# Optimization experiments

Hardware: AMD Instinct MI355X
Metric: run time of the kernel (lower is better)

Reference implementation:

```python
import jax, jax.numpy as jnp
import numpy as np

BN_EPS = 1e-5


def bn_relu(x, gamma, beta):
    # x: [N, C, L]; BatchNorm1d train-mode: per-channel stats over (N, L), biased var
    mean = jnp.mean(x, axis=(0, 2), keepdims=True)
    var = jnp.mean(jnp.square(x - mean), axis=(0, 2), keepdims=True)
    xn = (x - mean) * jax.lax.rsqrt(var + BN_EPS)
    return jax.nn.relu(xn * gamma[None, :, None] + beta[None, :, None])


def setup_inputs() -> dict:
    key = jax.random.key(0)
    ks = jax.random.split(key, 10)
    N, C, L = 8, 512, 2048
    IC = C // 2
    s = 0.02
    return {
        "A": jax.random.normal(ks[0], (N, C, L), jnp.float32),
        "B": jax.random.normal(ks[1], (N, C, L), jnp.float32),
        "bn_gamma": jnp.ones((C,), jnp.float32),
        "bn_beta": jnp.zeros((C,), jnp.float32),
        "theta_w": jax.random.normal(ks[2], (C, IC), jnp.float32) * s,
        "theta_b": jax.random.normal(ks[3], (IC,), jnp.float32) * s,
        "phi_w": jax.random.normal(ks[4], (C, IC), jnp.float32) * s,
        "phi_b": jax.random.normal(ks[5], (IC,), jnp.float32) * s,
        "g_w": jax.random.normal(ks[6], (C, IC), jnp.float32) * s,
        "g_b": jax.random.normal(ks[7], (IC,), jnp.float32) * s,
        "W_w": jax.random.normal(ks[8], (IC, C), jnp.float32) * s,
        "W_b": jax.random.normal(ks[9], (C,), jnp.float32) * s,
    }


def reference(A, B, bn_gamma, bn_beta, theta_w, theta_b, phi_w, phi_b, g_w, g_b, W_w, W_b):
    # A, B: [N, C, L]
    An = bn_relu(A, bn_gamma, bn_beta).transpose(0, 2, 1)  # [N, L, C]
    Bn = bn_relu(B, bn_gamma, bn_beta).transpose(0, 2, 1)  # [N, L, C]

    q = An @ theta_w + theta_b                 # [N, L, IC]
    k = Bn @ phi_w + phi_b                     # [N, L, IC]
    v = An @ g_w + g_b                         # [N, L, IC]

    scores = jnp.einsum("bnc,bmc->bnm", q, k)  # [N, L, L]  (no scaling in source)
    attn = jax.nn.softmax(scores, axis=-1)
    y = jnp.einsum("bnm,bmc->bnc", attn, v)    # [N, L, IC]

    out = An + (y @ W_w + W_b)                 # residual, [N, L, C]
    return out.transpose(0, 2, 1)              # [N, C, L]
```

## Files before the change

### kernel.cpp

```cpp
#include <hip/hip_runtime.h>

using bf16 = __bf16;
typedef __attribute__((ext_vector_type(8))) __bf16 bf16x8;
typedef __attribute__((ext_vector_type(4))) __bf16 bf16x4;
typedef __attribute__((ext_vector_type(4))) float f32x4;
typedef __attribute__((ext_vector_type(16))) float f32x16;
typedef __attribute__((ext_vector_type(4))) unsigned u32x4;
typedef __attribute__((ext_vector_type(2))) unsigned u32x2;

#define NB 8
#define CC 512
#define LL 2048
#define IC 256
#define NLTOT 16384
#define NSPLIT 4
#define BATCH_STRIDE 524288

__device__ inline bf16 f2bf(float f) {
    unsigned u = __builtin_bit_cast(unsigned, f);
    unsigned r = (u + 0x7fff + ((u >> 16) & 1)) >> 16;
    return __builtin_bit_cast(bf16, (unsigned short)r);
}
__device__ inline unsigned packbf(float lo, float hi) {
    unsigned a = (unsigned)__builtin_bit_cast(unsigned short, f2bf(lo));
    unsigned b = (unsigned)__builtin_bit_cast(unsigned short, f2bf(hi));
    return (b << 16) | a;
}

typedef const __attribute__((address_space(1))) void gas_void;
typedef __attribute__((address_space(3))) void las_void;

static constexpr size_t oScale = 0;
static constexpr size_t oWT    = 8192;
static constexpr size_t oAn    = oWT + 4ull * 262144;
static constexpr size_t oBn    = oAn + 16777216ull;
static constexpr size_t oQ     = oBn + 16777216ull;
static constexpr size_t oK     = oQ + 8388608ull;
static constexpr size_t oVT    = oK + 8388608ull;
static constexpr size_t oY     = oVT + 8388608ull;
static constexpr size_t oProj  = oY + 8388608ull;

__global__ __launch_bounds__(256) void prep_weights(
    const float* __restrict__ theta_w, const float* __restrict__ phi_w,
    const float* __restrict__ g_w, const float* __restrict__ W_w,
    bf16* __restrict__ wts)
{
    int idx = blockIdx.x * 256 + threadIdx.x;
    int which = idx >> 17;
    int o = idx & 131071;
    float v;
    if (which < 3) {
        const float* W = which == 0 ? theta_w : (which == 1 ? phi_w : g_w);
        int ic = o >> 9, cc = o & 511;
        v = W[cc * IC + ic];
    } else {
        int cc = o >> 8, ic = o & 255;
        v = W_w[ic * CC + cc];
    }
    wts[(size_t)which * 131072 + o] = f2bf(v);
}

__global__ __launch_bounds__(256) void bn_stats(
    const float* __restrict__ A, const float* __restrict__ B,
    const float* __restrict__ gamma, const float* __restrict__ beta,
    float* __restrict__ scaleshift)
{
    int bid = blockIdx.x;
    int tensor = bid >> 9, c = bid & 511;
    const float* X = tensor ? B : A;
    int t = threadIdx.x;
    float s = 0.f, sq = 0.f;
    for (int n = 0; n < NB; ++n) {
        const float* row = &X[((size_t)(n * CC + c)) << 11];
        for (int j = t * 4; j < LL; j += 1024) {
            float4 v = *(const float4*)&row[j];
            s += v.x + v.y + v.z + v.w;
            sq += v.x * v.x + v.y * v.y + v.z * v.z + v.w * v.w;
        }
    }
    __shared__ float rs[256], rq[256];
    rs[t] = s; rq[t] = sq;
    __syncthreads();
    for (int step = 128; step > 0; step >>= 1) {
        if (t < step) { rs[t] += rs[t + step]; rq[t] += rq[t + step]; }
        __syncthreads();
    }
    if (t == 0) {
        float mean = rs[0] * (1.f / 16384.f);
        float var = rq[0] * (1.f / 16384.f) - mean * mean;
        float rsq = rsqrtf(var + 1e-5f);
        float sc = gamma[c] * rsq;
        scaleshift[tensor * 1024 + c] = sc;
        scaleshift[tensor * 1024 + 512 + c] = beta[c] - mean * sc;
    }
}

__global__ __launch_bounds__(256) void bn_apply_transpose(
    const float* __restrict__ X, const float* __restrict__ scale,
    const float* __restrict__ shift, bf16* __restrict__ Out)
{
    int bidx = blockIdx.x;
    int lt = bidx & 31, ct = (bidx >> 5) & 7, n = bidx >> 8;
    int c0 = ct * 64, l0 = lt * 64;
    __shared__ float tile[64][65];
    int t = threadIdx.x;
    #pragma unroll
    for (int i = 0; i < 4; ++i) {
        int r = i * 16 + (t >> 4);
        int c4 = (t & 15) * 4;
        float s = scale[c0 + r], sh = shift[c0 + r];
        float4 v = *(const float4*)&X[(((size_t)n * CC + c0 + r) << 11) + l0 + c4];
        tile[r][c4 + 0] = fmaxf(v.x * s + sh, 0.f);
        tile[r][c4 + 1] = fmaxf(v.y * s + sh, 0.f);
        tile[r][c4 + 2] = fmaxf(v.z * s + sh, 0.f);
        tile[r][c4 + 3] = fmaxf(v.w * s + sh, 0.f);
    }
    __syncthreads();
    #pragma unroll
    for (int i = 0; i < 2; ++i) {
        int lr = i * 32 + (t >> 3);
        int c8 = (t & 7) * 8;
        bf16 tmp[8];
        #pragma unroll
        for (int e = 0; e < 8; ++e) tmp[e] = f2bf(tile[c8 + e][lr]);
        *(bf16x8*)&Out[(((size_t)(n << 11)) + l0 + lr) * CC + c0 + c8] = *(bf16x8*)tmp;
    }
}

__global__ __launch_bounds__(256) void gemm_qkv(
    const bf16* __restrict__ An, const bf16* __restrict__ Bn,
    const bf16* __restrict__ wts,
    const float* __restrict__ theta_b, const float* __restrict__ phi_b,
    const float* __restrict__ g_b,
    bf16* __restrict__ qB, bf16* __restrict__ kB, bf16* __restrict__ vB)
{
    int bid = blockIdx.x;
    int which = bid >> 8;
    int sub = bid & 255;
    const bf16* A  = (which == 1) ? Bn : An;
    const bf16* BT = wts + (size_t)which * 131072;
    const float* bias = which == 0 ? theta_b : (which == 1 ? phi_b : g_b);
    bf16* dst = which == 0 ? qB : (which == 1 ? kB : vB);

    int tn = sub & 1, tm = sub >> 1;
    int m0 = tm * 128, n0 = tn * 128;
    __shared__ bf16 a_lds[128][72];
    __shared__ bf16 b_lds[128][72];
    int t = threadIdx.x;
    int l = t & 63, w = t >> 6;
    int wr = w >> 1, wc = w & 1;
    f32x4 acc[4][4] = {};
    for (int k0 = 0; k0 < CC; k0 += 64) {
        __syncthreads();
        #pragma unroll
        for (int i = 0; i < 4; ++i) {
            int ci = t + i * 256;
            int row = ci >> 3, c8 = (ci & 7) * 8;
            *(bf16x8*)&a_lds[row][c8] = *(const bf16x8*)&A[(size_t)(m0 + row) * CC + k0 + c8];
            *(bf16x8*)&b_lds[row][c8] = *(const bf16x8*)&BT[(size_t)(n0 + row) * CC + k0 + c8];
        }
        __syncthreads();
        #pragma unroll
        for (int ks = 0; ks < 2; ++ks) {
            bf16x8 af[4], bfr[4];
            #pragma unroll
            for (int mi = 0; mi < 4; ++mi)
                af[mi] = *(const bf16x8*)&a_lds[wr * 64 + mi * 16 + (l & 15)][ks * 32 + (l >> 4) * 8];
            #pragma unroll
            for (int ni = 0; ni < 4; ++ni)
                bfr[ni] = *(const bf16x8*)&b_lds[wc * 64 + ni * 16 + (l & 15)][ks * 32 + (l >> 4) * 8];
            #pragma unroll
            for (int mi = 0; mi < 4; ++mi)
                #pragma unroll
                for (int ni = 0; ni < 4; ++ni)
                    acc[mi][ni] = __builtin_amdgcn_mfma_f32_16x16x32_bf16(af[mi], bfr[ni], acc[mi][ni], 0, 0, 0);
        }
    }
    #pragma unroll
    for (int mi = 0; mi < 4; ++mi)
        #pragma unroll
        for (int ni = 0; ni < 4; ++ni) {
            int col = n0 + wc * 64 + ni * 16 + (l & 15);
            float bv = bias[col];
            int row0 = m0 + wr * 64 + mi * 16 + (l >> 4) * 4;
            int nb = row0 >> 11;
            int li0 = row0 & 2047;
            size_t base = (size_t)nb * BATCH_STRIDE + (size_t)(li0 >> 5) * 8192;
            if (which < 2) {
                size_t a0 = base + (col >> 3) * 256 + (li0 & 31) * 8 + (col & 7);
                #pragma unroll
                for (int r = 0; r < 4; ++r)
                    dst[a0 + r * 8] = f2bf(acc[mi][ni][r] + bv);
            } else {
                bf16 tmp[4];
                #pragma unroll
                for (int r = 0; r < 4; ++r) tmp[r] = f2bf(acc[mi][ni][r] + bv);
                int kvin = li0 & 31;
                int grp = ((col >> 5) << 2) | ((kvin >> 4) << 1) | ((kvin >> 3) & 1);
                *(bf16x4*)&dst[base + grp * 256 + (col & 31) * 8 + (kvin & 7)] = *(bf16x4*)tmp;
            }
        }
}

__global__ __launch_bounds__(256) void gemm_w(
    const bf16* __restrict__ A, const bf16* __restrict__ BT,
    const float* __restrict__ bias, float* __restrict__ Cout,
    int Nn, int K, int nTilesN)
{
    int bid = blockIdx.x;
    int tn = bid % nTilesN, tm = bid / nTilesN;
    int m0 = tm * 128, n0 = tn * 128;
    __shared__ bf16 a_lds[128][72];
    __shared__ bf16 b_lds[128][72];
    int t = threadIdx.x;
    int l = t & 63, w = t >> 6;
    int wr = w >> 1, wc = w & 1;
    f32x4 acc[4][4] = {};
    for (int k0 = 0; k0 < K; k0 += 64) {
        __syncthreads();
        #pragma unroll
        for (int i = 0; i < 4; ++i) {
            int ci = t + i * 256;
            int row = ci >> 3, c8 = (ci & 7) * 8;
            *(bf16x8*)&a_lds[row][c8] = *(const bf16x8*)&A[(size_t)(m0 + row) * K + k0 + c8];
            *(bf16x8*)&b_lds[row][c8] = *(const bf16x8*)&BT[(size_t)(n0 + row) * K + k0 + c8];
        }
        __syncthreads();
        #pragma unroll
        for (int ks = 0; ks < 2; ++ks) {
            bf16x8 af[4], bfr[4];
            #pragma unroll
            for (int mi = 0; mi < 4; ++mi)
                af[mi] = *(const bf16x8*)&a_lds[wr * 64 + mi * 16 + (l & 15)][ks * 32 + (l >> 4) * 8];
            #pragma unroll
            for (int ni = 0; ni < 4; ++ni)
                bfr[ni] = *(const bf16x8*)&b_lds[wc * 64 + ni * 16 + (l & 15)][ks * 32 + (l >> 4) * 8];
            #pragma unroll
            for (int mi = 0; mi < 4; ++mi)
                #pragma unroll
                for (int ni = 0; ni < 4; ++ni)
                    acc[mi][ni] = __builtin_amdgcn_mfma_f32_16x16x32_bf16(af[mi], bfr[ni], acc[mi][ni], 0, 0, 0);
        }
    }
    #pragma unroll
    for (int mi = 0; mi < 4; ++mi)
        #pragma unroll
        for (int ni = 0; ni < 4; ++ni) {
            int col = n0 + wc * 64 + ni * 16 + (l & 15);
            float bv = bias[col];
            #pragma unroll
            for (int r = 0; r < 4; ++r) {
                int row = m0 + wr * 64 + mi * 16 + (l >> 4) * 4 + r;
                Cout[(size_t)row * Nn + col] = acc[mi][ni][r] + bv;
            }
        }
}

__global__ __launch_bounds__(256, 2) void flash_attn32(
    const bf16* __restrict__ QB, const bf16* __restrict__ KB,
    const bf16* __restrict__ VB, bf16* __restrict__ part, float* __restrict__ ml)
{
    int bid = blockIdx.x;
    int nb = bid & 7;
    int split = (bid >> 3) & 3;
    int qt = bid >> 5;
    int t = threadIdx.x, l = t & 63, w = t >> 6;
    int h = l >> 5, ql = l & 31;
    int qrow = qt * 128 + w * 32 + ql;
    const bf16* Qblk = QB + (size_t)nb * BATCH_STRIDE + (size_t)(qt * 4 + w) * 8192;
    const bf16* Kb = KB + (size_t)nb * BATCH_STRIDE;
    const bf16* Vb = VB + (size_t)nb * BATCH_STRIDE;

    __shared__ bf16 k_lds[2][8192];
    __shared__ bf16 v_lds[2][8192];

    int kb0 = split * 16;

    auto stage = [&](int buf, int blk) {
        const bf16* kg = Kb + (size_t)blk * 8192;
        const bf16* vg = Vb + (size_t)blk * 8192;
        #pragma unroll
        for (int i = 0; i < 4; ++i) {
            int e0 = (t + i * 256) * 8;
            __builtin_amdgcn_global_load_lds((gas_void*)(kg + e0),
                                             (las_void*)&k_lds[buf][e0], 16, 0, 0);
            __builtin_amdgcn_global_load_lds((gas_void*)(vg + e0),
                                             (las_void*)&v_lds[buf][e0], 16, 0, 0);
        }
    };

    stage(0, kb0);

    bf16x8 qf[16];
    #pragma unroll
    for (int dc = 0; dc < 16; ++dc)
        qf[dc] = *(const bf16x8*)&Qblk[(dc * 2 + h) * 256 + ql * 8];

    f32x16 o[8] = {};
    float m = -__builtin_inff(), ell = 0.f;

    __syncthreads();

    int buf = 0;
    for (int it = 0; it < 16; ++it) {
        if (it < 15) stage(buf ^ 1, kb0 + it + 1);

        f32x16 s = {};
        #pragma unroll
        for (int dc = 0; dc < 16; ++dc) {
            bf16x8 kf = *(const bf16x8*)&k_lds[buf][(dc * 2 + h) * 256 + ql * 8];
            s = __builtin_amdgcn_mfma_f32_32x32x16_bf16(kf, qf[dc], s, 0, 0, 0);
        }

        float tm = s[0];
        #pragma unroll
        for (int r = 1; r < 16; ++r) tm = fmaxf(tm, s[r]);
        tm = fmaxf(tm, __shfl_xor(tm, 32));
        if (!__all(tm <= m + 8.f)) {
            float nm = fmaxf(m, tm);
            float fac = __expf(m - nm);
            m = nm;
            ell *= fac;
            #pragma unroll
            for (int c = 0; c < 8; ++c)
                #pragma unroll
                for (int r = 0; r < 16; ++r) o[c][r] *= fac;
        }
        float ts = 0.f;
        #pragma unroll
        for (int r = 0; r < 16; ++r) { s[r] = __expf(s[r] - m); ts += s[r]; }
        ell += ts + __shfl_xor(ts, 32);

        unsigned wd[8], pw[8];
        #pragma unroll
        for (int j = 0; j < 8; ++j) wd[j] = packbf(s[2 * j], s[2 * j + 1]);
        #pragma unroll
        for (int j = 0; j < 8; ++j) pw[j] = __shfl_xor(wd[j], 32);
        u32x4 q0v = { h ? pw[2] : wd[0], h ? pw[3] : wd[1],
                      h ? wd[2] : pw[0], h ? wd[3] : pw[1] };
        u32x4 q1v = { h ? pw[6] : wd[4], h ? pw[7] : wd[5],
                      h ? wd[6] : pw[4], h ? wd[7] : pw[5] };
        bf16x8 pf0 = __builtin_bit_cast(bf16x8, q0v);
        bf16x8 pf1 = __builtin_bit_cast(bf16x8, q1v);

        #pragma unroll
        for (int c = 0; c < 8; ++c) {
            bf16x8 v0 = *(const bf16x8*)&v_lds[buf][(c * 4 + h) * 256 + ql * 8];
            bf16x8 v1 = *(const bf16x8*)&v_lds[buf][(c * 4 + 2 + h) * 256 + ql * 8];
            o[c] = __builtin_amdgcn_mfma_f32_32x32x16_bf16(v0, pf0, o[c], 0, 0, 0);
            o[c] = __builtin_amdgcn_mfma_f32_32x32x16_bf16(v1, pf1, o[c], 0, 0, 0);
        }

        __syncthreads();
        buf ^= 1;
    }

    size_t prow = (((size_t)split * NB + nb) << 11) + qrow;
    #pragma unroll
    for (int c = 0; c < 8; ++c)
        #pragma unroll
        for (int rq = 0; rq < 4; ++rq) {
            u32x2 u = { packbf(o[c][rq * 4 + 0], o[c][rq * 4 + 1]),
                        packbf(o[c][rq * 4 + 2], o[c][rq * 4 + 3]) };
            bf16x4 pv = __builtin_bit_cast(bf16x4, u);
            *(bf16x4*)&part[prow * IC + c * 32 + 8 * rq + 4 * h] = pv;
        }
    if (l < 32) {
        ml[prow * 2] = m;
        ml[prow * 2 + 1] = ell;
    }
}

__global__ __launch_bounds__(256) void attn_combine(
    const bf16* __restrict__ part, const float* __restrict__ ml, bf16* __restrict__ Y)
{
    int t = threadIdx.x;
    int rowg = blockIdx.x * 8 + (t >> 5);
    int lane = t & 31;
    float m[NSPLIT], lv[NSPLIT];
    float M = -__builtin_inff();
    #pragma unroll
    for (int s = 0; s < NSPLIT; ++s) {
        m[s] = ml[((size_t)s * NLTOT + rowg) * 2];
        lv[s] = ml[((size_t)s * NLTOT + rowg) * 2 + 1];
        M = fmaxf(M, m[s]);
    }
    float L = 0.f, wgt[NSPLIT];
    #pragma unroll
    for (int s = 0; s < NSPLIT; ++s) {
        wgt[s] = __expf(m[s] - M);
        L += lv[s] * wgt[s];
    }
    float invL = 1.0f / L;
    float acc[8] = {};
    #pragma unroll
    for (int s = 0; s < NSPLIT; ++s) {
        bf16x8 v = *(const bf16x8*)&part[((size_t)s * NLTOT + rowg) * IC + lane * 8];
        #pragma unroll
        for (int e = 0; e < 8; ++e) acc[e] += wgt[s] * (float)v[e];
    }
    bf16 outv[8];
    #pragma unroll
    for (int e = 0; e < 8; ++e) outv[e] = f2bf(acc[e] * invL);
    *(bf16x8*)&Y[(size_t)rowg * IC + lane * 8] = *(bf16x8*)outv;
}

__global__ __launch_bounds__(256) void final_out(
    const float* __restrict__ A, const float* __restrict__ scaleshift,
    const float* __restrict__ proj, float* __restrict__ Out)
{
    int bidx = blockIdx.x;
    int lt = bidx & 31, ct = (bidx >> 5) & 7, n = bidx >> 8;
    int c0 = ct * 64, l0 = lt * 64;
    __shared__ float tile[64][65];
    int t = threadIdx.x;
    #pragma unroll
    for (int i = 0; i < 4; ++i) {
        int lr = i * 16 + (t >> 4);
        int c4 = (t & 15) * 4;
        float4 v = *(const float4*)&proj[((((size_t)n) << 11) + l0 + lr) * CC + c0 + c4];
        tile[lr][c4 + 0] = v.x; tile[lr][c4 + 1] = v.y;
        tile[lr][c4 + 2] = v.z; tile[lr][c4 + 3] = v.w;
    }
    __syncthreads();
    #pragma unroll
    for (int i = 0; i < 4; ++i) {
        int cr = i * 16 + (t >> 4);
        int l4 = (t & 15) * 4;
        int c = c0 + cr;
        float s = scaleshift[c], sh = scaleshift[512 + c];
        float4 a = *(const float4*)&A[(((size_t)n * CC + c) << 11) + l0 + l4];
        float4 r;
        r.x = fmaxf(a.x * s + sh, 0.f) + tile[l4 + 0][cr];
        r.y = fmaxf(a.y * s + sh, 0.f) + tile[l4 + 1][cr];
        r.z = fmaxf(a.z * s + sh, 0.f) + tile[l4 + 2][cr];
        r.w = fmaxf(a.w * s + sh, 0.f) + tile[l4 + 3][cr];
        *(float4*)&Out[(((size_t)n * CC + c) << 11) + l0 + l4] = r;
    }
}

extern "C" void kernel_launch(void* const* d_in, const int* in_sizes, int n_in,
                              void* d_out, int out_size, void* d_ws, size_t ws_size,
                              hipStream_t stream) {
    const float* A       = (const float*)d_in[0];
    const float* B       = (const float*)d_in[1];
    const float* gamma   = (const float*)d_in[2];
    const float* beta    = (const float*)d_in[3];
    const float* theta_w = (const float*)d_in[4];
    const float* theta_b = (const float*)d_in[5];
    const float* phi_w   = (const float*)d_in[6];
    const float* phi_b   = (const float*)d_in[7];
    const float* g_w     = (const float*)d_in[8];
    const float* g_b     = (const float*)d_in[9];
    const float* W_w     = (const float*)d_in[10];
    const float* W_b     = (const float*)d_in[11];
    float* Out = (float*)d_out;

    char* ws = (char*)d_ws;
    float* scaleshift = (float*)(ws + oScale);
    bf16* wts    = (bf16*)(ws + oWT);
    bf16* WwT    = wts + 3 * 131072;
    bf16* An = (bf16*)(ws + oAn);
    bf16* Bn = (bf16*)(ws + oBn);
    bf16* qB = (bf16*)(ws + oQ);
    bf16* kB = (bf16*)(ws + oK);
    bf16* vB = (bf16*)(ws + oVT);
    bf16* y  = (bf16*)(ws + oY);
    float* proj = (float*)(ws + oProj);
    bf16* part = (bf16*)(ws + oAn);
    float* ml  = (float*)(ws + oProj);

    prep_weights<<<2048, 256, 0, stream>>>(theta_w, phi_w, g_w, W_w, wts);
    bn_stats<<<1024, 256, 0, stream>>>(A, B, gamma, beta, scaleshift);
    bn_apply_transpose<<<2048, 256, 0, stream>>>(A, scaleshift + 0,    scaleshift + 512,  An);
    bn_apply_transpose<<<2048, 256, 0, stream>>>(B, scaleshift + 1024, scaleshift + 1536, Bn);

    gemm_qkv<<<768, 256, 0, stream>>>(An, Bn, wts, theta_b, phi_b, g_b, qB, kB, vB);

    flash_attn32<<<128 * NSPLIT, 256, 0, stream>>>(qB, kB, vB, part, ml);
    attn_combine<<<2048, 256, 0, stream>>>(part, ml, y);

    gemm_w<<<512, 256, 0, stream>>>(y, WwT, W_b, proj, CC, IC, 4);

    final_out<<<2048, 256, 0, stream>>>(A, scaleshift, proj, Out);
}
```

Baseline: 150.7 us.

## Fuse output projection with BN-ReLU residual epilogue; add MFMA priority hints in attention

The W projection GEMM now writes straight into the [N,C,L] output, applying the BN-ReLU residual on A in its epilogue. This removes the separate final_out kernel and the fp32 proj round-trip through global memory. The flash attention loop wraps its MFMA sections in s_setprio and turns the row max and sum reductions into balanced trees to shorten dependency chains. The epilogue stores are float4 along L per channel, so the write pattern is strided across channels and may coalesce less well than the old LDS transpose.

```diff
diff --git a/kernel.cpp b/kernel.cpp
--- a/kernel.cpp
+++ b/kernel.cpp
@@ -202,13 +202,13 @@
         }
 }
 
-__global__ __launch_bounds__(256) void gemm_w(
-    const bf16* __restrict__ A, const bf16* __restrict__ BT,
-    const float* __restrict__ bias, float* __restrict__ Cout,
-    int Nn, int K, int nTilesN)
+__global__ __launch_bounds__(256) void gemm_w_fused(
+    const bf16* __restrict__ Ay, const bf16* __restrict__ BT,
+    const float* __restrict__ bias, const float* __restrict__ Aorig,
+    const float* __restrict__ scaleshift, float* __restrict__ Out)
 {
     int bid = blockIdx.x;
-    int tn = bid % nTilesN, tm = bid / nTilesN;
+    int tn = bid & 3, tm = bid >> 2;
     int m0 = tm * 128, n0 = tn * 128;
     __shared__ bf16 a_lds[128][72];
     __shared__ bf16 b_lds[128][72];
@@ -216,14 +216,14 @@
     int l = t & 63, w = t >> 6;
     int wr = w >> 1, wc = w & 1;
     f32x4 acc[4][4] = {};
-    for (int k0 = 0; k0 < K; k0 += 64) {
+    for (int k0 = 0; k0 < IC; k0 += 64) {
         __syncthreads();
         #pragma unroll
         for (int i = 0; i < 4; ++i) {
             int ci = t + i * 256;
             int row = ci >> 3, c8 = (ci & 7) * 8;
-            *(bf16x8*)&a_lds[row][c8] = *(const bf16x8*)&A[(size_t)(m0 + row) * K + k0 + c8];
-            *(bf16x8*)&b_lds[row][c8] = *(const bf16x8*)&BT[(size_t)(n0 + row) * K + k0 + c8];
+            *(bf16x8*)&a_lds[row][c8] = *(const bf16x8*)&Ay[(size_t)(m0 + row) * IC + k0 + c8];
+            *(bf16x8*)&b_lds[row][c8] = *(const bf16x8*)&BT[(size_t)(n0 + row) * IC + k0 + c8];
         }
         __syncthreads();
         #pragma unroll
@@ -242,18 +242,25 @@
                     acc[mi][ni] = __builtin_amdgcn_mfma_f32_16x16x32_bf16(af[mi], bfr[ni], acc[mi][ni], 0, 0, 0);
         }
     }
-    #pragma unroll
-    for (int mi = 0; mi < 4; ++mi)
-        #pragma unroll
-        for (int ni = 0; ni < 4; ++ni) {
-            int col = n0 + wc * 64 + ni * 16 + (l & 15);
-            float bv = bias[col];
-            #pragma unroll
-            for (int r = 0; r < 4; ++r) {
-                int row = m0 + wr * 64 + mi * 16 + (l >> 4) * 4 + r;
-                Cout[(size_t)row * Nn + col] = acc[mi][ni][r] + bv;
-            }
-        }
+    int nb = m0 >> 11;
+    #pragma unroll
+    for (int ni = 0; ni < 4; ++ni) {
+        int c = n0 + wc * 64 + ni * 16 + (l & 15);
+        float bv = bias[c];
+        float sc = scaleshift[c], sh = scaleshift[512 + c];
+        #pragma unroll
+        for (int mi = 0; mi < 4; ++mi) {
+            int li = (m0 & 2047) + wr * 64 + mi * 16 + (l >> 4) * 4;
+            size_t base = (((size_t)nb * CC + c) << 11) + li;
+            float4 a = *(const float4*)&Aorig[base];
+            float4 o;
+            o.x = fmaxf(a.x * sc + sh, 0.f) + acc[mi][ni][0] + bv;
+            o.y = fmaxf(a.y * sc + sh, 0.f) + acc[mi][ni][1] + bv;
+            o.z = fmaxf(a.z * sc + sh, 0.f) + acc[mi][ni][2] + bv;
+            o.w = fmaxf(a.w * sc + sh, 0.f) + acc[mi][ni][3] + bv;
+            *(float4*)&Out[base] = o;
+        }
+    }
 }
 
 __global__ __launch_bounds__(256, 2) void flash_attn32(
@@ -306,15 +313,19 @@
         if (it < 15) stage(buf ^ 1, kb0 + it + 1);
 
         f32x16 s = {};
+        __builtin_amdgcn_s_setprio(1);
         #pragma unroll
         for (int dc = 0; dc < 16; ++dc) {
             bf16x8 kf = *(const bf16x8*)&k_lds[buf][(dc * 2 + h) * 256 + ql * 8];
             s = __builtin_amdgcn_mfma_f32_32x32x16_bf16(kf, qf[dc], s, 0, 0, 0);
         }
-
-        float tm = s[0];
-        #pragma unroll
-        for (int r = 1; r < 16; ++r) tm = fmaxf(tm, s[r]);
+        __builtin_amdgcn_s_setprio(0);
+
+        float a0 = fmaxf(fmaxf(s[0], s[1]), fmaxf(s[2], s[3]));
+        float a1 = fmaxf(fmaxf(s[4], s[5]), fmaxf(s[6], s[7]));
+        float a2 = fmaxf(fmaxf(s[8], s[9]), fmaxf(s[10], s[11]));
+        float a3 = fmaxf(fmaxf(s[12], s[13]), fmaxf(s[14], s[15]));
+        float tm = fmaxf(fmaxf(a0, a1), fmaxf(a2, a3));
         tm = fmaxf(tm, __shfl_xor(tm, 32));
         if (!__all(tm <= m + 8.f)) {
             float nm = fmaxf(m, tm);
@@ -326,9 +337,13 @@
                 #pragma unroll
                 for (int r = 0; r < 16; ++r) o[c][r] *= fac;
         }
-        float ts = 0.f;
-        #pragma unroll
-        for (int r = 0; r < 16; ++r) { s[r] = __expf(s[r] - m); ts += s[r]; }
+        #pragma unroll
+        for (int r = 0; r < 16; ++r) s[r] = __expf(s[r] - m);
+        float t0 = (s[0] + s[1]) + (s[2] + s[3]);
+        float t1 = (s[4] + s[5]) + (s[6] + s[7]);
+        float t2 = (s[8] + s[9]) + (s[10] + s[11]);
+        float t3 = (s[12] + s[13]) + (s[14] + s[15]);
+        float ts = (t0 + t1) + (t2 + t3);
         ell += ts + __shfl_xor(ts, 32);
 
         unsigned wd[8], pw[8];
@@ -343,6 +358,7 @@
         bf16x8 pf0 = __builtin_bit_cast(bf16x8, q0v);
         bf16x8 pf1 = __builtin_bit_cast(bf16x8, q1v);
 
+        __builtin_amdgcn_s_setprio(1);
         #pragma unroll
         for (int c = 0; c < 8; ++c) {
             bf16x8 v0 = *(const bf16x8*)&v_lds[buf][(c * 4 + h) * 256 + ql * 8];
@@ -350,6 +366,7 @@
             o[c] = __builtin_amdgcn_mfma_f32_32x32x16_bf16(v0, pf0, o[c], 0, 0, 0);
             o[c] = __builtin_amdgcn_mfma_f32_32x32x16_bf16(v1, pf1, o[c], 0, 0, 0);
         }
+        __builtin_amdgcn_s_setprio(0);
 
         __syncthreads();
         buf ^= 1;
@@ -403,40 +420,6 @@
     #pragma unroll
     for (int e = 0; e < 8; ++e) outv[e] = f2bf(acc[e] * invL);
     *(bf16x8*)&Y[(size_t)rowg * IC + lane * 8] = *(bf16x8*)outv;
-}
-
-__global__ __launch_bounds__(256) void final_out(
-    const float* __restrict__ A, const float* __restrict__ scaleshift,
-    const float* __restrict__ proj, float* __restrict__ Out)
-{
-    int bidx = blockIdx.x;
-    int lt = bidx & 31, ct = (bidx >> 5) & 7, n = bidx >> 8;
-    int c0 = ct * 64, l0 = lt * 64;
-    __shared__ float tile[64][65];
-    int t = threadIdx.x;
-    #pragma unroll
-    for (int i = 0; i < 4; ++i) {
-        int lr = i * 16 + (t >> 4);
-        int c4 = (t & 15) * 4;
-        float4 v = *(const float4*)&proj[((((size_t)n) << 11) + l0 + lr) * CC + c0 + c4];
-        tile[lr][c4 + 0] = v.x; tile[lr][c4 + 1] = v.y;
-        tile[lr][c4 + 2] = v.z; tile[lr][c4 + 3] = v.w;
-    }
-    __syncthreads();
-    #pragma unroll
-    for (int i = 0; i < 4; ++i) {
-        int cr = i * 16 + (t >> 4);
-        int l4 = (t & 15) * 4;
-        int c = c0 + cr;
-        float s = scaleshift[c], sh = scaleshift[512 + c];
-        float4 a = *(const float4*)&A[(((size_t)n * CC + c) << 11) + l0 + l4];
-        float4 r;
-        r.x = fmaxf(a.x * s + sh, 0.f) + tile[l4 + 0][cr];
-        r.y = fmaxf(a.y * s + sh, 0.f) + tile[l4 + 1][cr];
-        r.z = fmaxf(a.z * s + sh, 0.f) + tile[l4 + 2][cr];
-        r.w = fmaxf(a.w * s + sh, 0.f) + tile[l4 + 3][cr];
-        *(float4*)&Out[(((size_t)n * CC + c) << 11) + l0 + l4] = r;
-    }
 }
 
 extern "C" void kernel_launch(void* const* d_in, const int* in_sizes, int n_in,
@@ -466,7 +449,6 @@
     bf16* kB = (bf16*)(ws + oK);
     bf16* vB = (bf16*)(ws + oVT);
     bf16* y  = (bf16*)(ws + oY);
-    float* proj = (float*)(ws + oProj);
     bf16* part = (bf16*)(ws + oAn);
     float* ml  = (float*)(ws + oProj);
 
@@ -480,7 +462,5 @@
     flash_attn32<<<128 * NSPLIT, 256, 0, stream>>>(qB, kB, vB, part, ml);
     attn_combine<<<2048, 256, 0, stream>>>(part, ml, y);
 
-    gemm_w<<<512, 256, 0, stream>>>(y, WwT, W_b, proj, CC, IC, 4);
-
-    final_out<<<2048, 256, 0, stream>>>(A, scaleshift, proj, Out);
-}
+    gemm_w_fused<<<512, 256, 0, stream>>>(y, WwT, W_b, A, scaleshift, Out);
+}
```

New measurement: 145.4 us. 1.04x faster.
